# Kernel tuning notes

Hardware: AMD Instinct MI355X
Metric: run time of the kernel (lower is better)

Reference implementation:

```python
import jax, jax.numpy as jnp
import numpy as np

D_K = 128
SCALER = np.sqrt(D_K).astype(np.float32)

def setup_inputs() -> dict:
    key = jax.random.key(0)
    kq, kk, kv = jax.random.split(key, 3)
    B, L, D = 16, 2048, D_K
    q = jax.random.normal(kq, (B, L, D), dtype=jnp.float32)
    k = jax.random.normal(kk, (B, L, D), dtype=jnp.float32)
    v = jax.random.normal(kv, (B, L, D), dtype=jnp.float32)
    return {"q": q, "k": k, "v": v}

def reference(q, k, v):
    # score[b, i, j] = q[b, i, :] . k[b, j, :] / sqrt(d_k)
    score = jnp.einsum('bid,bjd->bij', q, k) / SCALER
    attn = jax.nn.softmax(score, axis=-1)
    # output[b, i, :] = sum_j attn[b, i, j] * v[b, j, :]
    return jnp.einsum('bij,bjd->bid', attn, v)
```

## Files before the change

kernel.cpp:

```cpp
#include <hip/hip_runtime.h>
#include <stdint.h>


typedef short bf16x8 __attribute__((ext_vector_type(8)));
typedef float f32x4 __attribute__((ext_vector_type(4)));
typedef unsigned int u32;
typedef unsigned short u16;

#define L_SEQ  2048
#define D_HEAD 128
#define TSZ    8388608u
#define W_PART (2u * TSZ)
#define W_LSUM (W_PART + 768u * 32768u)
#define WS_NEED (W_LSUM + 768u * 128u * 4u)

__device__ __forceinline__ unsigned pk2(float lo, float hi) {
    union { float f; unsigned u; } a, b;
    a.f = lo; b.f = hi;
    return __builtin_amdgcn_perm(b.u + 0x8000u, a.u + 0x8000u, 0x07060302u);
}
__device__ __forceinline__ float ex2(float x) { return __builtin_amdgcn_exp2f(x); }
__device__ __forceinline__ float bflo(unsigned w) {
    union { unsigned u; float f; } v; v.u = w << 16; return v.f;
}
__device__ __forceinline__ float bfhi(unsigned w) {
    union { unsigned u; float f; } v; v.u = w & 0xffff0000u; return v.f;
}
__device__ __forceinline__ void gl_lds16(const u16* g, u16* l) {
    __builtin_amdgcn_global_load_lds(
        (const __attribute__((address_space(1))) u32*)g,
        (__attribute__((address_space(3))) u32*)l, 16, 0, 0);
}

__global__ __launch_bounds__(256, 4)
void prepass(const float* __restrict__ K, const float* __restrict__ V,
             u16* __restrict__ kb, u16* __restrict__ vt) {
    const int id = blockIdx.x, t = threadIdx.x;
    if (id < 512) {
        const float* src = K + (size_t)id * 64 * 128;
        u16*        dst = kb + (size_t)id * 64 * 128;
        const int r = t >> 2;
        #pragma unroll
        for (int i = 0; i < 4; ++i) {
            int gp = (t & 3) * 4 + i;
            int gs = gp ^ (r & 7);
            const float* s = src + r * 128 + gs * 8;
            float4 x0 = *(const float4*)s, x1 = *(const float4*)(s + 4);
            uint4 w;
            w.x = pk2(x0.x, x0.y); w.y = pk2(x0.z, x0.w);
            w.z = pk2(x1.x, x1.y); w.w = pk2(x1.z, x1.w);
            *(uint4*)(dst + r * 128 + gp * 8) = w;
        }
    } else {
        __shared__ __align__(16) u16 vl[128 * 72];
        const int bid = id - 512;
        const float* src = V + (size_t)bid * 64 * 128;
        const int vcc = t & 31, vgk = t >> 5;
        union { float4 v; float f[4]; } vr[8];
        const float* vp = src + (size_t)(vgk * 8) * 128 + vcc * 4;
        #pragma unroll
        for (int r = 0; r < 8; ++r) vr[r].v = *(const float4*)(vp + (size_t)r * 128);
        #pragma unroll
        for (int dd = 0; dd < 4; ++dd) {
            uint4 w;
            w.x = pk2(vr[0].f[dd], vr[1].f[dd]);
            w.y = pk2(vr[2].f[dd], vr[3].f[dd]);
            w.z = pk2(vr[4].f[dd], vr[5].f[dd]);
            w.w = pk2(vr[6].f[dd], vr[7].f[dd]);
            *(uint4*)(&vl[(vcc * 4 + dd) * 72 + vgk * 8]) = w;
        }
        __syncthreads();
        u16* dst = vt + (size_t)bid * 8192;
        #pragma unroll
        for (int i = 0; i < 4; ++i) {
            int flat = t + 256 * i;
            int d = flat >> 3, gp = flat & 7;
            uint4 w = *(const uint4*)(&vl[d * 72 + ((gp ^ (d & 7)) * 8)]);
            *(uint4*)(dst + (size_t)flat * 8) = w;
        }
    }
}

__global__ __launch_bounds__(256, 2)
void attn2(const float* __restrict__ Qg, const u16* __restrict__ kb,
           const u16* __restrict__ vt, u16* __restrict__ part,
           float* __restrict__ lsum) {
    __shared__ __align__(16) char smem[73728];
    const int tid = threadIdx.x;
    const int wv = tid >> 6, lane = tid & 63;
    const int c = lane & 15, qd = lane >> 4, cx = c & 7;
    const int bid = blockIdx.x;
    const int p = bid & 255, kvh = bid >> 8;
    const int b = p & 15, qblk = p >> 4;
    const int t0 = kvh * 16;
    const int nt = 16;

    const float* Qp = Qg + (size_t)b * L_SEQ * D_HEAD;
    const u16*   Kp = kb + (size_t)b * L_SEQ * D_HEAD + (size_t)t0 * 8192;
    const u16*   Vp = vt + (size_t)b * 32 * 8192 + (size_t)t0 * 8192;
    u16* Pl = (u16*)(smem + 65536) + wv * 1024;

    const int so = wv * 2048 + lane * 8;
    const int psw = (c & 7) << 1;

    {
        u16* K0 = (u16*)smem;
        u16* V0 = (u16*)(smem + 32768);
        #pragma unroll
        for (int i = 0; i < 4; ++i) {
            gl_lds16(Kp + so + i * 512, K0 + so + i * 512);
            gl_lds16(Vp + so + i * 512, V0 + so + i * 512);
        }
    }

    const float QS = 1.4426950408889634f / 11.313708498984761f;
    bf16x8 qf[2][4];
    #pragma unroll
    for (int s = 0; s < 2; ++s) {
        const float* qrow = Qp + (size_t)(qblk * 128 + wv * 32 + s * 16 + c) * 128 + qd * 8;
        #pragma unroll
        for (int kt = 0; kt < 4; ++kt) {
            float4 x0 = *(const float4*)(qrow + kt * 32);
            float4 x1 = *(const float4*)(qrow + kt * 32 + 4);
            union { unsigned u[4]; bf16x8 v; } tt;
            tt.u[0] = pk2(x0.x * QS, x0.y * QS);
            tt.u[1] = pk2(x0.z * QS, x0.w * QS);
            tt.u[2] = pk2(x1.x * QS, x1.y * QS);
            tt.u[3] = pk2(x1.z * QS, x1.w * QS);
            qf[s][kt] = tt.v;
        }
    }

    f32x4 acc[2][8];
    #pragma unroll
    for (int s = 0; s < 2; ++s)
        #pragma unroll
        for (int dt = 0; dt < 8; ++dt) acc[s][dt] = (f32x4){0.f, 0.f, 0.f, 0.f};
    float lrun[2] = {0.f, 0.f};

    __syncthreads();

    #pragma unroll 2
    for (int it = 0; it < nt; ++it) {
        u16* Kc = (u16*)(smem + ((it & 1) << 14));
        u16* Vc = (u16*)(smem + 32768 + ((it & 1) << 14));

        if (it + 1 < nt) {
            u16* Kn = (u16*)(smem + ((~it & 1) << 14));
            u16* Vn = (u16*)(smem + 32768 + ((~it & 1) << 14));
            const u16* kg = Kp + (size_t)(it + 1) * 8192 + so;
            const u16* vg = Vp + (size_t)(it + 1) * 8192 + so;
            #pragma unroll
            for (int i = 0; i < 4; ++i) {
                gl_lds16(kg + i * 512, Kn + so + i * 512);
                gl_lds16(vg + i * 512, Vn + so + i * 512);
            }
        }

        f32x4 st[4][2];
        #pragma unroll
        for (int v = 0; v < 4; ++v) {
            st[v][0] = (f32x4){0.f, 0.f, 0.f, 0.f};
            st[v][1] = (f32x4){0.f, 0.f, 0.f, 0.f};
        }
        #pragma unroll
        for (int kt = 0; kt < 4; ++kt) {
            const int g = ((kt * 4 + qd) ^ cx) * 8;
            #pragma unroll
            for (int v = 0; v < 4; ++v) {
                bf16x8 a = *(const bf16x8*)(Kc + (v * 16 + c) * 128 + g);
                st[v][0] = __builtin_amdgcn_mfma_f32_16x16x32_bf16(a, qf[0][kt], st[v][0], 0, 0, 0);
                st[v][1] = __builtin_amdgcn_mfma_f32_16x16x32_bf16(a, qf[1][kt], st[v][1], 0, 0, 0);
            }
        }

        bf16x8 pf[2][2];
        #pragma unroll
        for (int s = 0; s < 2; ++s) {
            float lsm = 0.f;
            #pragma unroll
            for (int v = 0; v < 4; ++v) {
                float p0 = ex2(st[v][s].x), p1 = ex2(st[v][s].y);
                float p2 = ex2(st[v][s].z), p3 = ex2(st[v][s].w);
                lsm += (p0 + p1) + (p2 + p3);
                uint2 w; w.x = pk2(p0, p1); w.y = pk2(p2, p3);
                int gsw = (v * 4 + qd) ^ psw;
                *(uint2*)(Pl + c * 64 + gsw * 4) = w;
            }
            lrun[s] += lsm;
            #pragma unroll
            for (int h = 0; h < 2; ++h) {
                int gsw = (h * 8 + qd * 2) ^ psw;
                pf[h][s] = *(const bf16x8*)(Pl + c * 64 + gsw * 4);
            }
            if (s == 0) asm volatile("s_waitcnt lgkmcnt(0)" ::: "memory");
        }

        #pragma unroll
        for (int dt = 0; dt < 8; ++dt) {
            #pragma unroll
            for (int h = 0; h < 2; ++h) {
                bf16x8 a = *(const bf16x8*)(Vc + (dt * 16 + c) * 64 + ((h * 4 + qd) ^ cx) * 8);
                acc[0][dt] = __builtin_amdgcn_mfma_f32_16x16x32_bf16(a, pf[h][0], acc[0][dt], 0, 0, 0);
                acc[1][dt] = __builtin_amdgcn_mfma_f32_16x16x32_bf16(a, pf[h][1], acc[1][dt], 0, 0, 0);
            }
        }

        if (it + 1 < nt) __syncthreads();
    }

    float ls[2];
    #pragma unroll
    for (int s = 0; s < 2; ++s) {
        float l = lrun[s];
        l += __shfl_xor(l, 16);
        l += __shfl_xor(l, 32);
        ls[s] = l;
    }
    u16* pb = part + (size_t)bid * 16384;
    #pragma unroll
    for (int s = 0; s < 2; ++s)
        #pragma unroll
        for (int dt = 0; dt < 8; ++dt) {
            f32x4 o = acc[s][dt];
            uint2 w; w.x = pk2(o.x, o.y); w.y = pk2(o.z, o.w);
            *(uint2*)(pb + ((((wv * 2 + s) * 8 + dt) * 64 + lane) << 2)) = w;
        }
    if (qd == 0) {
        lsum[kvh * 32768 + p * 128 + wv * 32 + c]      = ls[0];
        lsum[kvh * 32768 + p * 128 + wv * 32 + 16 + c] = ls[1];
    }
}

__global__ __launch_bounds__(256, 2)
void combine2(const u16* __restrict__ part, const float* __restrict__ lsum,
              float* __restrict__ Og) {
    __shared__ float inv[128];
    __shared__ __align__(16) float Ol[64 * 132];
    const int t = threadIdx.x, p = blockIdx.x;
    const int b = p & 15, qblk = p >> 4;
    if (t < 128) {
        float l0 = lsum[p * 128 + t];
        float l1 = lsum[32768 + p * 128 + t];
        inv[t] = 1.0f / (l0 + l1);
    }
    const uint2* P0 = (const uint2*)(part + (size_t)p * 16384);
    const uint2* P1 = (const uint2*)(part + (size_t)(256 + p) * 16384);
    __syncthreads();
    #pragma unroll
    for (int h = 0; h < 2; ++h) {
        #pragma unroll
        for (int i = 0; i < 8; ++i) {
            int slot = i * 256 + t;
            int lc = slot >> 6, lane = slot & 63;
            int gc = h * 32 + lc;
            int s = (lc >> 3) & 1, dt = lc & 7;
            int qd = lane >> 4, cc = lane & 15;
            int row = (lc >> 4) * 32 + s * 16 + cc;
            int d0 = dt * 16 + qd * 4;
            size_t idx = (size_t)gc * 64 + lane;
            uint2 w0 = P0[idx], w1 = P1[idx];
            float iv = inv[h * 64 + row];
            float4 o;
            o.x = (bflo(w0.x) + bflo(w1.x)) * iv;
            o.y = (bfhi(w0.x) + bfhi(w1.x)) * iv;
            o.z = (bflo(w0.y) + bflo(w1.y)) * iv;
            o.w = (bfhi(w0.y) + bfhi(w1.y)) * iv;
            *(float4*)(&Ol[row * 132 + d0]) = o;
        }
        __syncthreads();
        #pragma unroll
        for (int i = 0; i < 8; ++i) {
            int slot = i * 256 + t;
            int row = slot >> 5, c4 = slot & 31;
            float4 val = *(const float4*)(&Ol[row * 132 + c4 * 4]);
            size_t q = (size_t)b * L_SEQ + qblk * 128 + h * 64 + row;
            *(float4*)(Og + q * D_HEAD + c4 * 4) = val;
        }
        __syncthreads();
    }
}

extern "C" void kernel_launch(void* const* d_in, const int* in_sizes, int n_in,
                              void* d_out, int out_size, void* d_ws, size_t ws_size,
                              hipStream_t stream) {
    const float* q = (const float*)d_in[0];
    const float* k = (const float*)d_in[1];
    const float* v = (const float*)d_in[2];
    float* out = (float*)d_out;
    u16* kb = (u16*)d_ws;
    u16* vt = (u16*)((char*)d_ws + TSZ);
    u16* part = (u16*)((char*)d_ws + W_PART);
    float* ls = (float*)((char*)d_ws + W_LSUM);
    prepass<<<dim3(1024), dim3(256), 0, stream>>>(k, v, kb, vt);
    attn2<<<dim3(512), dim3(256), 0, stream>>>(q, kb, vt, part, ls);
    combine2<<<dim3(256), dim3(256), 0, stream>>>(part, ls, out);
}
```

Baseline: 137.6 us.

## Fuse K/V conversion, attention, and combine into one single-pass kernel

Replaces the three-kernel pipeline (K/V bf16 prepass, split-KV attention, combine) with one kernel of 256 blocks of 512 threads. Each block converts fp32 K/V tiles to bf16 in registers and LDS while computing the current tile. Two wave groups split each KV tile and reduce their partial outputs through LDS. This removes the workspace round-trips and extra launches, but the grid drops to 256 blocks and the loop gains more barriers and in-loop conversion work.

```diff
diff --git a/kernel.cpp b/kernel.cpp
--- a/kernel.cpp
+++ b/kernel.cpp
@@ -9,10 +9,15 @@
 
 #define L_SEQ  2048
 #define D_HEAD 128
-#define TSZ    8388608u
-#define W_PART (2u * TSZ)
-#define W_LSUM (W_PART + 768u * 32768u)
-#define WS_NEED (W_LSUM + 768u * 128u * 4u)
+#define NT     32
+
+#define OFF_K   0
+#define OFF_V   32768
+#define OFF_VL  65536
+#define OFF_P   83968
+#define OFF_LS  100352
+#define OFF_INV 100864
+#define LDS_SZ  101376
 
 __device__ __forceinline__ unsigned pk2(float lo, float hi) {
     union { float f; unsigned u; } a, b;
@@ -20,104 +25,90 @@
     return __builtin_amdgcn_perm(b.u + 0x8000u, a.u + 0x8000u, 0x07060302u);
 }
 __device__ __forceinline__ float ex2(float x) { return __builtin_amdgcn_exp2f(x); }
-__device__ __forceinline__ float bflo(unsigned w) {
-    union { unsigned u; float f; } v; v.u = w << 16; return v.f;
-}
-__device__ __forceinline__ float bfhi(unsigned w) {
-    union { unsigned u; float f; } v; v.u = w & 0xffff0000u; return v.f;
-}
-__device__ __forceinline__ void gl_lds16(const u16* g, u16* l) {
-    __builtin_amdgcn_global_load_lds(
-        (const __attribute__((address_space(1))) u32*)g,
-        (__attribute__((address_space(3))) u32*)l, 16, 0, 0);
-}
-
-__global__ __launch_bounds__(256, 4)
-void prepass(const float* __restrict__ K, const float* __restrict__ V,
-             u16* __restrict__ kb, u16* __restrict__ vt) {
-    const int id = blockIdx.x, t = threadIdx.x;
-    if (id < 512) {
-        const float* src = K + (size_t)id * 64 * 128;
-        u16*        dst = kb + (size_t)id * 64 * 128;
-        const int r = t >> 2;
-        #pragma unroll
-        for (int i = 0; i < 4; ++i) {
-            int gp = (t & 3) * 4 + i;
-            int gs = gp ^ (r & 7);
-            const float* s = src + r * 128 + gs * 8;
-            float4 x0 = *(const float4*)s, x1 = *(const float4*)(s + 4);
-            uint4 w;
-            w.x = pk2(x0.x, x0.y); w.y = pk2(x0.z, x0.w);
-            w.z = pk2(x1.x, x1.y); w.w = pk2(x1.z, x1.w);
-            *(uint4*)(dst + r * 128 + gp * 8) = w;
-        }
-    } else {
-        __shared__ __align__(16) u16 vl[128 * 72];
-        const int bid = id - 512;
-        const float* src = V + (size_t)bid * 64 * 128;
-        const int vcc = t & 31, vgk = t >> 5;
-        union { float4 v; float f[4]; } vr[8];
-        const float* vp = src + (size_t)(vgk * 8) * 128 + vcc * 4;
-        #pragma unroll
-        for (int r = 0; r < 8; ++r) vr[r].v = *(const float4*)(vp + (size_t)r * 128);
-        #pragma unroll
-        for (int dd = 0; dd < 4; ++dd) {
-            uint4 w;
-            w.x = pk2(vr[0].f[dd], vr[1].f[dd]);
-            w.y = pk2(vr[2].f[dd], vr[3].f[dd]);
-            w.z = pk2(vr[4].f[dd], vr[5].f[dd]);
-            w.w = pk2(vr[6].f[dd], vr[7].f[dd]);
-            *(uint4*)(&vl[(vcc * 4 + dd) * 72 + vgk * 8]) = w;
-        }
-        __syncthreads();
-        u16* dst = vt + (size_t)bid * 8192;
-        #pragma unroll
-        for (int i = 0; i < 4; ++i) {
-            int flat = t + 256 * i;
-            int d = flat >> 3, gp = flat & 7;
-            uint4 w = *(const uint4*)(&vl[d * 72 + ((gp ^ (d & 7)) * 8)]);
-            *(uint4*)(dst + (size_t)flat * 8) = w;
-        }
-    }
-}
-
-__global__ __launch_bounds__(256, 2)
-void attn2(const float* __restrict__ Qg, const u16* __restrict__ kb,
-           const u16* __restrict__ vt, u16* __restrict__ part,
-           float* __restrict__ lsum) {
-    __shared__ __align__(16) char smem[73728];
+
+__global__ __launch_bounds__(512, 2)
+void attn_fused(const float* __restrict__ Qg, const float* __restrict__ Kg,
+                const float* __restrict__ Vg, float* __restrict__ Og) {
+    __shared__ __align__(16) char smem[LDS_SZ];
     const int tid = threadIdx.x;
     const int wv = tid >> 6, lane = tid & 63;
     const int c = lane & 15, qd = lane >> 4, cx = c & 7;
-    const int bid = blockIdx.x;
-    const int p = bid & 255, kvh = bid >> 8;
-    const int b = p & 15, qblk = p >> 4;
-    const int t0 = kvh * 16;
-    const int nt = 16;
-
+    const int wl = wv & 3, wg = wv >> 2;
+    const int p = blockIdx.x;
+    const int b = p >> 4, qblk = p & 15;
     const float* Qp = Qg + (size_t)b * L_SEQ * D_HEAD;
-    const u16*   Kp = kb + (size_t)b * L_SEQ * D_HEAD + (size_t)t0 * 8192;
-    const u16*   Vp = vt + (size_t)b * 32 * 8192 + (size_t)t0 * 8192;
-    u16* Pl = (u16*)(smem + 65536) + wv * 1024;
-
-    const int so = wv * 2048 + lane * 8;
-    const int psw = (c & 7) << 1;
-
-    {
-        u16* K0 = (u16*)smem;
-        u16* V0 = (u16*)(smem + 32768);
-        #pragma unroll
-        for (int i = 0; i < 4; ++i) {
-            gl_lds16(Kp + so + i * 512, K0 + so + i * 512);
-            gl_lds16(Vp + so + i * 512, V0 + so + i * 512);
-        }
-    }
+    const float* Kp = Kg + (size_t)b * L_SEQ * D_HEAD;
+    const float* Vp = Vg + (size_t)b * L_SEQ * D_HEAD;
+
+    u16* Pl = (u16*)(smem + OFF_P) + wv * 1024;
+    const int psw = cx << 1;
+
+    const int vcc = tid & 31, vgk = (tid >> 5) & 7;
+    union { float4 v; float f[4]; } stg[8];
+
+    auto stage_load = [&](int tile) {
+        if (wg == 0) {
+            const float* base = Kp + (size_t)tile * 64 * 128;
+            #pragma unroll
+            for (int i = 0; i < 4; ++i) {
+                int r = wl * 16 + i * 4 + (lane >> 4);
+                int g = lane & 15;
+                stg[2*i].v   = *(const float4*)(base + r * 128 + g * 8);
+                stg[2*i+1].v = *(const float4*)(base + r * 128 + g * 8 + 4);
+            }
+        } else {
+            const float* base = Vp + (size_t)(tile * 64 + vgk * 8) * 128 + vcc * 4;
+            #pragma unroll
+            for (int r = 0; r < 8; ++r)
+                stg[r].v = *(const float4*)(base + (size_t)r * 128);
+        }
+    };
+    auto stage_write = [&](int buf) {
+        if (wg == 0) {
+            u16* Kd = (u16*)(smem + OFF_K) + buf * 8192;
+            #pragma unroll
+            for (int i = 0; i < 4; ++i) {
+                int r = wl * 16 + i * 4 + (lane >> 4);
+                int g = lane & 15;
+                uint4 w;
+                w.x = pk2(stg[2*i].f[0],   stg[2*i].f[1]);
+                w.y = pk2(stg[2*i].f[2],   stg[2*i].f[3]);
+                w.z = pk2(stg[2*i+1].f[0], stg[2*i+1].f[1]);
+                w.w = pk2(stg[2*i+1].f[2], stg[2*i+1].f[3]);
+                *(uint4*)(Kd + r * 128 + ((g ^ (r & 7)) * 8)) = w;
+            }
+        } else {
+            u16* vl = (u16*)(smem + OFF_VL);
+            #pragma unroll
+            for (int dd = 0; dd < 4; ++dd) {
+                uint4 w;
+                w.x = pk2(stg[0].f[dd], stg[1].f[dd]);
+                w.y = pk2(stg[2].f[dd], stg[3].f[dd]);
+                w.z = pk2(stg[4].f[dd], stg[5].f[dd]);
+                w.w = pk2(stg[6].f[dd], stg[7].f[dd]);
+                *(uint4*)(vl + (vcc * 4 + dd) * 72 + vgk * 8) = w;
+            }
+        }
+    };
+    auto phase_b = [&](int buf) {
+        const u16* vl = (const u16*)(smem + OFF_VL);
+        u16* Vd = (u16*)(smem + OFF_V) + buf * 8192;
+        #pragma unroll
+        for (int i = 0; i < 2; ++i) {
+            int flat = tid + 512 * i;
+            int d = flat >> 3, gp = flat & 7;
+            uint4 w = *(const uint4*)(vl + d * 72 + ((gp ^ (d & 7)) * 8));
+            *(uint4*)(Vd + d * 64 + gp * 8) = w;
+        }
+    };
+
+    stage_load(0);
 
     const float QS = 1.4426950408889634f / 11.313708498984761f;
     bf16x8 qf[2][4];
     #pragma unroll
     for (int s = 0; s < 2; ++s) {
-        const float* qrow = Qp + (size_t)(qblk * 128 + wv * 32 + s * 16 + c) * 128 + qd * 8;
+        const float* qrow = Qp + (size_t)(qblk * 128 + wl * 32 + s * 16 + c) * 128 + qd * 8;
         #pragma unroll
         for (int kt = 0; kt < 4; ++kt) {
             float4 x0 = *(const float4*)(qrow + kt * 32);
@@ -131,6 +122,11 @@
         }
     }
 
+    stage_write(0);
+    __syncthreads();
+    phase_b(0);
+    __syncthreads();
+
     f32x4 acc[2][8];
     #pragma unroll
     for (int s = 0; s < 2; ++s)
@@ -138,28 +134,17 @@
         for (int dt = 0; dt < 8; ++dt) acc[s][dt] = (f32x4){0.f, 0.f, 0.f, 0.f};
     float lrun[2] = {0.f, 0.f};
 
-    __syncthreads();
-
     #pragma unroll 2
-    for (int it = 0; it < nt; ++it) {
-        u16* Kc = (u16*)(smem + ((it & 1) << 14));
-        u16* Vc = (u16*)(smem + 32768 + ((it & 1) << 14));
-
-        if (it + 1 < nt) {
-            u16* Kn = (u16*)(smem + ((~it & 1) << 14));
-            u16* Vn = (u16*)(smem + 32768 + ((~it & 1) << 14));
-            const u16* kg = Kp + (size_t)(it + 1) * 8192 + so;
-            const u16* vg = Vp + (size_t)(it + 1) * 8192 + so;
-            #pragma unroll
-            for (int i = 0; i < 4; ++i) {
-                gl_lds16(kg + i * 512, Kn + so + i * 512);
-                gl_lds16(vg + i * 512, Vn + so + i * 512);
-            }
-        }
-
-        f32x4 st[4][2];
-        #pragma unroll
-        for (int v = 0; v < 4; ++v) {
+    for (int it = 0; it < NT; ++it) {
+        const int cur = it & 1;
+        if (it + 1 < NT) stage_load(it + 1);
+
+        const u16* Kc = (const u16*)(smem + OFF_K) + cur * 8192;
+        const u16* Vc = (const u16*)(smem + OFF_V) + cur * 8192;
+
+        f32x4 st[2][2];
+        #pragma unroll
+        for (int v = 0; v < 2; ++v) {
             st[v][0] = (f32x4){0.f, 0.f, 0.f, 0.f};
             st[v][1] = (f32x4){0.f, 0.f, 0.f, 0.f};
         }
@@ -167,19 +152,19 @@
         for (int kt = 0; kt < 4; ++kt) {
             const int g = ((kt * 4 + qd) ^ cx) * 8;
             #pragma unroll
-            for (int v = 0; v < 4; ++v) {
-                bf16x8 a = *(const bf16x8*)(Kc + (v * 16 + c) * 128 + g);
+            for (int v = 0; v < 2; ++v) {
+                bf16x8 a = *(const bf16x8*)(Kc + (wg * 32 + v * 16 + c) * 128 + g);
                 st[v][0] = __builtin_amdgcn_mfma_f32_16x16x32_bf16(a, qf[0][kt], st[v][0], 0, 0, 0);
                 st[v][1] = __builtin_amdgcn_mfma_f32_16x16x32_bf16(a, qf[1][kt], st[v][1], 0, 0, 0);
             }
         }
 
-        bf16x8 pf[2][2];
+        bf16x8 pf[2];
         #pragma unroll
         for (int s = 0; s < 2; ++s) {
             float lsm = 0.f;
             #pragma unroll
-            for (int v = 0; v < 4; ++v) {
+            for (int v = 0; v < 2; ++v) {
                 float p0 = ex2(st[v][s].x), p1 = ex2(st[v][s].y);
                 float p2 = ex2(st[v][s].z), p3 = ex2(st[v][s].w);
                 lsm += (p0 + p1) + (p2 + p3);
@@ -188,25 +173,24 @@
                 *(uint2*)(Pl + c * 64 + gsw * 4) = w;
             }
             lrun[s] += lsm;
-            #pragma unroll
-            for (int h = 0; h < 2; ++h) {
-                int gsw = (h * 8 + qd * 2) ^ psw;
-                pf[h][s] = *(const bf16x8*)(Pl + c * 64 + gsw * 4);
-            }
+            int gsw2 = (qd * 2) ^ psw;
+            pf[s] = *(const bf16x8*)(Pl + c * 64 + gsw2 * 4);
             if (s == 0) asm volatile("s_waitcnt lgkmcnt(0)" ::: "memory");
         }
 
         #pragma unroll
         for (int dt = 0; dt < 8; ++dt) {
-            #pragma unroll
-            for (int h = 0; h < 2; ++h) {
-                bf16x8 a = *(const bf16x8*)(Vc + (dt * 16 + c) * 64 + ((h * 4 + qd) ^ cx) * 8);
-                acc[0][dt] = __builtin_amdgcn_mfma_f32_16x16x32_bf16(a, pf[h][0], acc[0][dt], 0, 0, 0);
-                acc[1][dt] = __builtin_amdgcn_mfma_f32_16x16x32_bf16(a, pf[h][1], acc[1][dt], 0, 0, 0);
-            }
-        }
-
-        if (it + 1 < nt) __syncthreads();
+            bf16x8 a = *(const bf16x8*)(Vc + (dt * 16 + c) * 64 + ((wg * 4 + qd) ^ cx) * 8);
+            acc[0][dt] = __builtin_amdgcn_mfma_f32_16x16x32_bf16(a, pf[0], acc[0][dt], 0, 0, 0);
+            acc[1][dt] = __builtin_amdgcn_mfma_f32_16x16x32_bf16(a, pf[1], acc[1][dt], 0, 0, 0);
+        }
+
+        if (it + 1 < NT) {
+            stage_write(1 - cur);
+            __syncthreads();
+            phase_b(1 - cur);
+            __syncthreads();
+        }
     }
 
     float ls[2];
@@ -217,82 +201,70 @@
         l += __shfl_xor(l, 32);
         ls[s] = l;
     }
-    u16* pb = part + (size_t)bid * 16384;
-    #pragma unroll
-    for (int s = 0; s < 2; ++s)
-        #pragma unroll
-        for (int dt = 0; dt < 8; ++dt) {
-            f32x4 o = acc[s][dt];
-            uint2 w; w.x = pk2(o.x, o.y); w.y = pk2(o.z, o.w);
-            *(uint2*)(pb + ((((wv * 2 + s) * 8 + dt) * 64 + lane) << 2)) = w;
-        }
-    if (qd == 0) {
-        lsum[kvh * 32768 + p * 128 + wv * 32 + c]      = ls[0];
-        lsum[kvh * 32768 + p * 128 + wv * 32 + 16 + c] = ls[1];
-    }
-}
-
-__global__ __launch_bounds__(256, 2)
-void combine2(const u16* __restrict__ part, const float* __restrict__ lsum,
-              float* __restrict__ Og) {
-    __shared__ float inv[128];
-    __shared__ __align__(16) float Ol[64 * 132];
-    const int t = threadIdx.x, p = blockIdx.x;
-    const int b = p & 15, qblk = p >> 4;
-    if (t < 128) {
-        float l0 = lsum[p * 128 + t];
-        float l1 = lsum[32768 + p * 128 + t];
-        inv[t] = 1.0f / (l0 + l1);
-    }
-    const uint2* P0 = (const uint2*)(part + (size_t)p * 16384);
-    const uint2* P1 = (const uint2*)(part + (size_t)(256 + p) * 16384);
-    __syncthreads();
-    #pragma unroll
-    for (int h = 0; h < 2; ++h) {
-        #pragma unroll
-        for (int i = 0; i < 8; ++i) {
-            int slot = i * 256 + t;
-            int lc = slot >> 6, lane = slot & 63;
-            int gc = h * 32 + lc;
-            int s = (lc >> 3) & 1, dt = lc & 7;
-            int qd = lane >> 4, cc = lane & 15;
-            int row = (lc >> 4) * 32 + s * 16 + cc;
-            int d0 = dt * 16 + qd * 4;
-            size_t idx = (size_t)gc * 64 + lane;
-            uint2 w0 = P0[idx], w1 = P1[idx];
-            float iv = inv[h * 64 + row];
-            float4 o;
-            o.x = (bflo(w0.x) + bflo(w1.x)) * iv;
-            o.y = (bfhi(w0.x) + bfhi(w1.x)) * iv;
-            o.z = (bflo(w0.y) + bflo(w1.y)) * iv;
-            o.w = (bfhi(w0.y) + bfhi(w1.y)) * iv;
-            *(float4*)(&Ol[row * 132 + d0]) = o;
-        }
-        __syncthreads();
-        #pragma unroll
-        for (int i = 0; i < 8; ++i) {
-            int slot = i * 256 + t;
-            int row = slot >> 5, c4 = slot & 31;
-            float4 val = *(const float4*)(&Ol[row * 132 + c4 * 4]);
-            size_t q = (size_t)b * L_SEQ + qblk * 128 + h * 64 + row;
-            *(float4*)(Og + q * D_HEAD + c4 * 4) = val;
-        }
-        __syncthreads();
+    __syncthreads();
+    if (wg == 1) {
+        f32x4* lin = (f32x4*)(smem + wl * 16384);
+        #pragma unroll
+        for (int s = 0; s < 2; ++s)
+            #pragma unroll
+            for (int dt = 0; dt < 8; ++dt)
+                lin[(s * 8 + dt) * 64 + lane] = acc[s][dt];
+        float* lsl = (float*)(smem + OFF_LS);
+        if (qd == 0) {
+            lsl[wl * 32 + c]      = ls[0];
+            lsl[wl * 32 + 16 + c] = ls[1];
+        }
+    }
+    __syncthreads();
+    if (wg == 0) {
+        const f32x4* lin = (const f32x4*)(smem + wl * 16384);
+        const float* lsl = (const float*)(smem + OFF_LS);
+        float* invl = (float*)(smem + OFF_INV);
+        #pragma unroll
+        for (int s = 0; s < 2; ++s)
+            #pragma unroll
+            for (int dt = 0; dt < 8; ++dt)
+                acc[s][dt] += lin[(s * 8 + dt) * 64 + lane];
+        float l0 = ls[0] + lsl[wl * 32 + c];
+        float l1 = ls[1] + lsl[wl * 32 + 16 + c];
+        if (qd == 0) {
+            invl[wl * 32 + c]      = 1.0f / l0;
+            invl[wl * 32 + 16 + c] = 1.0f / l1;
+        }
+    }
+    __syncthreads();
+    if (wg == 0) {
+        float* Ow = (float*)smem + wl * 4224;
+        #pragma unroll
+        for (int s = 0; s < 2; ++s)
+            #pragma unroll
+            for (int dt = 0; dt < 8; ++dt)
+                *(f32x4*)(&Ow[(s * 16 + c) * 132 + dt * 16 + qd * 4]) = acc[s][dt];
+    }
+    __syncthreads();
+    {
+        const float* Ow = (const float*)smem + wl * 4224;
+        const float* invl = (const float*)(smem + OFF_INV);
+        #pragma unroll
+        for (int j = 0; j < 8; ++j) {
+            int quad = (wg * 8 + j) * 64 + lane;
+            int row = quad >> 5, c4 = quad & 31;
+            f32x4 o = *(const f32x4*)(&Ow[row * 132 + c4 * 4]);
+            float iv = invl[wl * 32 + row];
+            o.x *= iv; o.y *= iv; o.z *= iv; o.w *= iv;
+            size_t qr = (size_t)b * L_SEQ + qblk * 128 + wl * 32 + row;
+            *(f32x4*)(Og + qr * D_HEAD + c4 * 4) = o;
+        }
     }
 }
 
 extern "C" void kernel_launch(void* const* d_in, const int* in_sizes, int n_in,
                               void* d_out, int out_size, void* d_ws, size_t ws_size,
                               hipStream_t stream) {
+    (void)d_ws; (void)ws_size; (void)in_sizes; (void)n_in; (void)out_size;
     const float* q = (const float*)d_in[0];
     const float* k = (const float*)d_in[1];
     const float* v = (const float*)d_in[2];
     float* out = (float*)d_out;
-    u16* kb = (u16*)d_ws;
-    u16* vt = (u16*)((char*)d_ws + TSZ);
-    u16* part = (u16*)((char*)d_ws + W_PART);
-    float* ls = (float*)((char*)d_ws + W_LSUM);
-    prepass<<<dim3(1024), dim3(256), 0, stream>>>(k, v, kb, vt);
-    attn2<<<dim3(512), dim3(256), 0, stream>>>(q, kb, vt, part, ls);
-    combine2<<<dim3(256), dim3(256), 0, stream>>>(part, ls, out);
+    attn_fused<<<dim3(256), dim3(512), 0, stream>>>(q, k, v, out);
 }
```

Result: slower. 244.0 us (+77.4%).
